# Kernel tuning notes

Measured on AMD Instinct MI355X. Metric: run time of the kernel, lower is better.

## Reference

```python
import jax, jax.numpy as jnp
import numpy as np

EPS = 1e-8
H, DH = 4, 8
HID = H * DH  # 32
FF = 20       # 4 * dim
C = 5         # channels per degree


def snorm(x):
    # grad-safe L2 norm over last axis
    return jnp.sqrt(jnp.sum(x * x, axis=-1) + 1e-12)


def _ln(v, gamma, beta):
    mu = v.mean(-1, keepdims=True)
    sd = v.std(-1, keepdims=True) + EPS
    return (v - mu) / sd * gamma + beta


def norm_se3(x0, x1, g, b):
    # equivariant norm: transform per-channel invariant norms, keep orientation (phase)
    n0 = jnp.abs(x0)
    y0 = jnp.sign(x0) * jax.nn.gelu(_ln(n0, g[0], b[0]))
    n1 = snorm(x1)                                        # (b,n,c)
    y1 = x1 / n1[..., None] * jax.nn.gelu(_ln(n1, g[1], b[1]))[..., None]
    return y0, y1


def attention(x0, x1, coors, adjm, Wq, Mk, Mv, R1, rb1, R2, rb2, Wo0, Wo1):
    b, n, c = x0.shape
    rel = coors[:, None, :, :] - coors[:, :, None, :]     # (b,i,j,3): x_j - x_i
    dist = jnp.sqrt(jnp.sum(rel * rel, -1, keepdims=True) + 1e-12)
    u = rel / dist                                        # unit directions
    # radial net -> per-edge kernel coefficients for each degree-pair/basis (k and v)
    phi = jax.nn.relu(dist @ R1 + rb1) @ R2 + rb2         # (b,i,j,12*HID)
    (k00, k10, k01, kI, kU, kX, v00, v10, v01, vI, vU, vX) = jnp.split(phi, 12, -1)

    def edge_feats(M, p00, p10, p01, pI, pU, pX):
        y00 = jnp.einsum('bjc,ch->bjh', x0, M[0])
        y10 = jnp.einsum('bjcm,ch->bjhm', x1, M[1])
        y01 = jnp.einsum('bjc,ch->bjh', x0, M[2])
        yI = jnp.einsum('bjcm,ch->bjhm', x1, M[3])
        yU = jnp.einsum('bjcm,ch->bjhm', x1, M[4])
        yX = jnp.einsum('bjcm,ch->bjhm', x1, M[5])
        # degree-0 messages: (0->0) scalar and (1->0) vector.dot(u) paths
        e0 = p00 * y00[:, None] + p10 * jnp.einsum('bjhm,bijm->bijh', y10, u)
        un = u[:, :, :, None, :]                          # (b,i,j,1,3)
        # degree-1 messages: closed-form equivariant bases u*s, I, u(u.v), u x v
        e1 = (p01[..., None] * y01[:, None, :, :, None] * un
              + pI[..., None] * yI[:, None]
              + pU[..., None] * jnp.einsum('bjhm,bijm->bijh', yU, u)[..., None] * un
              + pX[..., None] * jnp.cross(un, yX[:, None]))
        return e0, e1

    k0, k1 = edge_feats(Mk, k00, k10, k01, kI, kU, kX)
    v0, v1 = edge_feats(Mv, v00, v10, v01, vI, vU, vX)

    q0 = jnp.einsum('bic,ch->bih', x0, Wq[0]).reshape(b, n, H, DH)
    q1 = jnp.einsum('bicm,ch->bihm', x1, Wq[1]).reshape(b, n, H, DH, 3)
    logits = (jnp.einsum('bihd,bijhd->bhij', q0, k0.reshape(b, n, n, H, DH))
              + jnp.einsum('bihdm,bijhdm->bhij', q1, k1.reshape(b, n, n, H, DH, 3)))
    logits = logits / jnp.asarray(DH, x0.dtype) ** 0.5
    logits = jnp.where(adjm[:, None], logits, -1e9)       # sparse-neighbor mask
    attn = jax.nn.softmax(logits, axis=-1)
    o0 = jnp.einsum('bhij,bijhd->bihd', attn, v0.reshape(b, n, n, H, DH)).reshape(b, n, HID)
    o1 = jnp.einsum('bhij,bijhdm->bihdm', attn, v1.reshape(b, n, n, H, DH, 3)).reshape(b, n, HID, 3)
    return o0 @ Wo0, jnp.einsum('bnhm,hc->bncm', o1, Wo1)


def feedforward(x0, x1, Wf1, Wf2, gs, bs):
    h0 = jax.nn.gelu(jnp.einsum('bnc,cf->bnf', x0, Wf1[0]))
    h1 = jnp.einsum('bncm,cf->bnfm', x1, Wf1[1])
    h1 = h1 * jax.nn.sigmoid(snorm(h1) * gs + bs)[..., None]   # norm-gated nonlin (equivariant)
    return jnp.einsum('bnf,fc->bnc', h0, Wf2[0]), jnp.einsum('bnfm,fc->bncm', h1, Wf2[1])


def _forward(feats, coors, adj_mat, Wq, Mk, Mv, R1, rb1, R2, rb2, Wo0, Wo1, gnA, bnA, gnF, bnF, Wf1, Wf2, gs, bs, Wh1, bh1, Wh2, bh2):
    b, n, _ = feats.shape
    a = adj_mat.astype(jnp.float32)
    # num_adj_degrees=2: attend over 1-hop OR 2-hop neighbors (plus self)
    adjm = adj_mat | ((a @ a) > 0) | jnp.eye(n, dtype=bool)
    x0 = feats
    x1 = jnp.zeros(feats.shape + (3,), feats.dtype)       # input fiber has only degree-0
    x0n, x1n = norm_se3(x0, x1, gnA, bnA)
    d0, d1 = attention(x0n, x1n, coors, adjm, Wq, Mk, Mv, R1, rb1, R2, rb2, Wo0, Wo1)
    x0, x1 = x0 + d0, x1 + d1
    x0n, x1n = norm_se3(x0, x1, gnF, bnF)
    f0, f1 = feedforward(x0n, x1n, Wf1, Wf2, gs, bs)
    x0, x1 = x0 + f0, x1 + f1
    pooled = x0.mean(axis=1)                              # mean pool type-0 features
    h = jax.nn.relu(pooled @ Wh1 + bh1)
    out = h @ Wh2 + bh2                                   # (b, 9)
    return out.reshape(-1, 3, 3)


def setup_inputs():
    key = jax.random.key(0)
    ks = jax.random.split(key, 16)
    B, N = 2, 256
    g = lambda i, shape, s: jax.random.normal(ks[i], shape, jnp.float32) * s
    feats = g(0, (B, N, C), 1.0)
    coors = g(1, (B, N, 3), 3.0)
    r = jax.random.uniform(ks[2], (B, N, N))
    adj = r < 0.03
    adj = (adj | jnp.swapaxes(adj, 1, 2)) & ~jnp.eye(N, dtype=bool)
    s5, sh, sf, s128 = C ** -0.5, HID ** -0.5, FF ** -0.5, 128 ** -0.5
    return dict(
        feats=feats, coors=coors, adj_mat=adj,
        Wq=g(3, (2, C, HID), s5), Mk=g(4, (6, C, HID), s5), Mv=g(5, (6, C, HID), s5),
        R1=g(6, (1, 32), 1.0), rb1=jnp.zeros(32), R2=g(7, (32, 12 * HID), 32 ** -0.5), rb2=jnp.zeros(12 * HID),
        Wo0=g(8, (HID, C), sh), Wo1=g(9, (HID, C), sh),
        gnA=jnp.ones((2, C)), bnA=jnp.zeros((2, C)), gnF=jnp.ones((2, C)), bnF=jnp.zeros((2, C)),
        Wf1=g(10, (2, C, FF), s5), Wf2=g(11, (2, FF, C), sf), gs=jnp.ones(FF), bs=jnp.zeros(FF),
        Wh1=g(12, (C, 128), s5), bh1=jnp.zeros(128), Wh2=g(13, (128, 9), s128), bh2=jnp.zeros(9))


def reference(feats, coors, adj_mat, Wq, Mk, Mv, R1, rb1, R2, rb2, Wo0, Wo1, gnA, bnA, gnF, bnF, Wf1, Wf2, gs, bs, Wh1, bh1, Wh2, bh2):
    return _forward(feats, coors, adj_mat, Wq, Mk, Mv, R1, rb1, R2, rb2, Wo0, Wo1, gnA, bnA, gnF, bnF, Wf1, Wf2, gs, bs, Wh1, bh1, Wh2, bh2)
```

## Files before the change

kernel.cpp:

```cpp
#include <hip/hip_runtime.h>
#include <math.h>

#define BB 2
#define NN 256
#define CC 5
#define HIDD 32


__device__ __forceinline__ float gelu_tanh(float x) {
    float x3 = x * x * x;
    return 0.5f * x * (1.0f + tanhf(0.7978845608028654f * (x + 0.044715f * x3)));
}
__device__ __forceinline__ float sgnf(float x) {
    return (x > 0.f) ? 1.f : ((x < 0.f) ? -1.f : 0.f);
}

#define TROW 9
#define TSZ (33 * TROW)

__global__ __launch_bounds__(256) void prep(
    const int* __restrict__ adj,
    const float* __restrict__ feats,
    const float* __restrict__ Wq0, const float* __restrict__ Mk0, const float* __restrict__ Mv0,
    const float* __restrict__ gnA0, const float* __restrict__ bnA0,
    const float* __restrict__ R1, const float* __restrict__ rb1,
    const float* __restrict__ R2, const float* __restrict__ rb2,
    unsigned long long* __restrict__ bits,
    float* __restrict__ q0, float* __restrict__ yk, float* __restrict__ yv,
    float* __restrict__ table,
    float* __restrict__ tsg)
{
    int bid = blockIdx.x;
    int tid = threadIdx.x;

    if (bid < 128) {
        int lane = tid & 63, wave = tid >> 6;
        int row = bid * 4 + wave;
#pragma unroll
        for (int k = 0; k < 4; k++) {
            int v = adj[(size_t)row * NN + k * 64 + lane];
            unsigned long long m = __ballot(v != 0);
            if (lane == 0) bits[row * 4 + k] = m;
        }
    } else if (bid < 192) {
        int node = (bid - 128) * 8 + (tid >> 5);
        int hd = tid & 31;
        const float* f = feats + node * CC;
        float n0[CC], x0n[CC];
        float mu = 0.f;
#pragma unroll
        for (int c = 0; c < CC; c++) { n0[c] = fabsf(f[c]); mu += n0[c]; }
        mu *= (1.0f / CC);
        float var = 0.f;
#pragma unroll
        for (int c = 0; c < CC; c++) { float d = n0[c] - mu; var += d * d; }
        var *= (1.0f / CC);
        float sd = sqrtf(var) + 1e-8f;
#pragma unroll
        for (int c = 0; c < CC; c++) {
            float ln = (n0[c] - mu) / sd * gnA0[c] + bnA0[c];
            x0n[c] = sgnf(f[c]) * gelu_tanh(ln);
        }
        float q = 0.f, k = 0.f, v = 0.f;
#pragma unroll
        for (int c = 0; c < CC; c++) {
            q = fmaf(x0n[c], Wq0[c * HIDD + hd], q);
            k = fmaf(x0n[c], Mk0[c * HIDD + hd], k);
            v = fmaf(x0n[c], Mv0[c * HIDD + hd], v);
        }
        q0[node * HIDD + hd] = q;
        yk[node * HIDD + hd] = k;
        yv[node * HIDD + hd] = v;
    } else {
        __shared__ float sR1[32], srb1[32], tt[32], ts[32], reps[33];
        if (tid < 32) { sR1[tid] = R1[tid]; srb1[tid] = rb1[tid]; }
        __syncthreads();
        if (tid < 32) {
            float r = sR1[tid];
            tt[tid] = (r != 0.f) ? (-srb1[tid] / r) : -3.0e38f;
        }
        __syncthreads();
        if (tid < 32) {
            float t = tt[tid];
            int rank = 0;
            for (int k = 0; k < 32; k++) {
                float tk = tt[k];
                rank += (tk < t) || (tk == t && k < tid);
            }
            ts[rank] = t;
        }
        __syncthreads();
        if (tid < 33) {
            float rep;
            if (tid == 0) rep = ts[0] - 1.0f;
            else if (tid == 32) rep = ts[31] + 1.0f;
            else rep = 0.5f * (ts[tid - 1] + ts[tid]);
            reps[tid] = rep;
            if (tid < 32) tsg[tid] = ts[tid];
        }
        __syncthreads();
        for (int idx = tid; idx < 33 * 32; idx += 256) {
            int p = idx >> 5, hd = idx & 31;
            float rep = reps[p];
            float A = 0.f, Bv = 0.f, Cv = 0.f, Dv = 0.f;
            for (int w = 0; w < 32; w++) {
                float r = sR1[w], bb = srb1[w];
                if (fmaf(r, rep, bb) > 0.f) {
                    float rk = R2[w * 384 + hd];
                    float rv = R2[w * 384 + 192 + hd];
                    A = fmaf(r, rk, A); Bv = fmaf(bb, rk, Bv);
                    Cv = fmaf(r, rv, Cv); Dv = fmaf(bb, rv, Dv);
                }
            }
            Bv += rb2[hd];
            Dv += rb2[192 + hd];
            table[0 * 33 * 36 + p * 36 + hd] = A;
            table[1 * 33 * 36 + p * 36 + hd] = Bv;
            table[2 * 33 * 36 + p * 36 + hd] = Cv;
            table[3 * 33 * 36 + p * 36 + hd] = Dv;
        }
    }
}

__global__ __launch_bounds__(256) void edge_attn(
    const float* __restrict__ coors,
    const float* __restrict__ q0g, const float* __restrict__ ykg, const float* __restrict__ yvg,
    const unsigned long long* __restrict__ bits,
    const float* __restrict__ feats,
    const float* __restrict__ Wo0,
    const float* __restrict__ gnF0, const float* __restrict__ bnF0,
    const float* __restrict__ Wf10,
    const float* __restrict__ Wf20,
    const float* __restrict__ table, const float* __restrict__ tsg,
    float* __restrict__ xfin)
{
    int node = blockIdx.x;
    int b = node >> 8, i = node & 255;
    int tid = threadIdx.x;
    int j = tid;
    int lane = tid & 63, wave = tid >> 6;

    __shared__ float4 sT[4 * TSZ];
    __shared__ float sts[32], q0s[32];
    __shared__ float Wo0t[5][32];
    __shared__ unsigned long long sbits[4];
    __shared__ float wredm[4][4], wreds[4][4], hm[4], hs[4];
    __shared__ float ew[4][5], x0as[5], xfs[5], h0s[20];

    {
        const float4* tg = (const float4*)table;
        for (int idx = tid; idx < 4 * TSZ; idx += 256) sT[idx] = tg[idx];
    }
    if (tid < 32) { sts[tid] = tsg[tid]; q0s[tid] = q0g[node * 32 + tid]; }
    if (tid < 160) Wo0t[tid / 32][tid % 32] = Wo0[(tid % 32) * 5 + tid / 32];
    if (tid < 4) sbits[tid] = bits[node * 4 + tid];
    __syncthreads();

    float dx = coors[(b * NN + j) * 3 + 0] - coors[(b * NN + i) * 3 + 0];
    float dy = coors[(b * NN + j) * 3 + 1] - coors[(b * NN + i) * 3 + 1];
    float dz = coors[(b * NN + j) * 3 + 2] - coors[(b * NN + i) * 3 + 2];
    float dist = sqrtf(dx * dx + dy * dy + dz * dz + 1e-12f);

    int p = 0;
#pragma unroll
    for (int k = 0; k < 32; k++) p += (sts[k] < dist) ? 1 : 0;

    const float4* Ap = sT + 0 * TSZ + p * TROW;
    const float4* Bp = sT + 1 * TSZ + p * TROW;
    const float4* Cp = sT + 2 * TSZ + p * TROW;
    const float4* Dp = sT + 3 * TSZ + p * TROW;
    const float4* ykp = (const float4*)(ykg + (size_t)(b * NN + j) * 32);
    const float4* yvp = (const float4*)(yvg + (size_t)(b * NN + j) * 32);
    const float4* q04 = (const float4*)q0s;

    float lg[4] = {0.f, 0.f, 0.f, 0.f};
#pragma unroll
    for (int q = 0; q < 8; q++) {
        float4 a = Ap[q], bb = Bp[q], y = ykp[q], qq = q04[q];
        int h = q >> 1;
        lg[h] = fmaf(fmaf(dist, a.x, bb.x) * qq.x, y.x, lg[h]);
        lg[h] = fmaf(fmaf(dist, a.y, bb.y) * qq.y, y.y, lg[h]);
        lg[h] = fmaf(fmaf(dist, a.z, bb.z) * qq.z, y.z, lg[h]);
        lg[h] = fmaf(fmaf(dist, a.w, bb.w) * qq.w, y.w, lg[h]);
    }

    {
        const unsigned long long* myb = bits + (size_t)(b * NN + j) * 4;
        bool direct = (sbits[j >> 6] >> (j & 63)) & 1ull;
        unsigned long long shr = (sbits[0] & myb[0]) | (sbits[1] & myb[1]) |
                                 (sbits[2] & myb[2]) | (sbits[3] & myb[3]);
        bool ok = direct || (shr != 0ull) || (i == j);
        const float invs = 0.35355339059327379f;
#pragma unroll
        for (int h = 0; h < 4; h++) lg[h] = ok ? lg[h] * invs : -1e9f;
    }

    float attn[4];
#pragma unroll
    for (int h = 0; h < 4; h++) {
        float v = lg[h];
        for (int off = 32; off; off >>= 1) v = fmaxf(v, __shfl_xor(v, off, 64));
        if (lane == 0) wredm[h][wave] = v;
    }
    __syncthreads();
    if (tid < 4) hm[tid] = fmaxf(fmaxf(wredm[tid][0], wredm[tid][1]), fmaxf(wredm[tid][2], wredm[tid][3]));
    __syncthreads();
#pragma unroll
    for (int h = 0; h < 4; h++) lg[h] = expf(lg[h] - hm[h]);
#pragma unroll
    for (int h = 0; h < 4; h++) {
        float v = lg[h];
        for (int off = 32; off; off >>= 1) v += __shfl_xor(v, off, 64);
        if (lane == 0) wreds[h][wave] = v;
    }
    __syncthreads();
    if (tid < 4) hs[tid] = wreds[tid][0] + wreds[tid][1] + wreds[tid][2] + wreds[tid][3];
    __syncthreads();
#pragma unroll
    for (int h = 0; h < 4; h++) attn[h] = lg[h] / hs[h];

    float e[5] = {0.f, 0.f, 0.f, 0.f, 0.f};
#pragma unroll
    for (int q = 0; q < 8; q++) {
        float4 c4 = Cp[q], d4 = Dp[q], y = yvp[q];
        float at = attn[q >> 1];
        float4 pv;
        pv.x = at * fmaf(dist, c4.x, d4.x) * y.x;
        pv.y = at * fmaf(dist, c4.y, d4.y) * y.y;
        pv.z = at * fmaf(dist, c4.z, d4.z) * y.z;
        pv.w = at * fmaf(dist, c4.w, d4.w) * y.w;
#pragma unroll
        for (int c = 0; c < 5; c++) {
            float4 w4 = ((const float4*)Wo0t[c])[q];
            e[c] = fmaf(pv.x, w4.x, fmaf(pv.y, w4.y, fmaf(pv.z, w4.z, fmaf(pv.w, w4.w, e[c]))));
        }
    }
    for (int off = 32; off; off >>= 1)
#pragma unroll
        for (int c = 0; c < 5; c++) e[c] += __shfl_xor(e[c], off, 64);
    if (lane == 0)
#pragma unroll
        for (int c = 0; c < 5; c++) ew[wave][c] = e[c];
    __syncthreads();

    if (tid < 5) {
        float d0 = ew[0][tid] + ew[1][tid] + ew[2][tid] + ew[3][tid];
        x0as[tid] = feats[node * 5 + tid] + d0;
    }
    __syncthreads();
    if (tid < 5) {
        float x0a[5], n0[5];
        float mu = 0.f;
#pragma unroll
        for (int c = 0; c < 5; c++) { x0a[c] = x0as[c]; n0[c] = fabsf(x0a[c]); mu += n0[c]; }
        mu *= 0.2f;
        float var = 0.f;
#pragma unroll
        for (int c = 0; c < 5; c++) { float d = n0[c] - mu; var += d * d; }
        var *= 0.2f;
        float sd = sqrtf(var) + 1e-8f;
        float ln = (n0[tid] - mu) / sd * gnF0[tid] + bnF0[tid];
        xfs[tid] = sgnf(x0a[tid]) * gelu_tanh(ln);
    }
    __syncthreads();
    if (tid < 20) {
        float s = 0.f;
#pragma unroll
        for (int c = 0; c < 5; c++) s = fmaf(xfs[c], Wf10[c * 20 + tid], s);
        h0s[tid] = gelu_tanh(s);
    }
    __syncthreads();
    if (tid < 5) {
        float f0 = 0.f;
        for (int f = 0; f < 20; f++) f0 = fmaf(h0s[f], Wf20[f * 5 + tid], f0);
        xfin[node * 5 + tid] = x0as[tid] + f0;
    }
}

__global__ __launch_bounds__(256) void head_mlp(const float* __restrict__ xfin,
                         const float* __restrict__ Wh1, const float* __restrict__ bh1,
                         const float* __restrict__ Wh2, const float* __restrict__ bh2,
                         float* __restrict__ out) {
    __shared__ float part[2][5][25];
    __shared__ float pooled[10];
    __shared__ float hdn[2][128];
    int tid = threadIdx.x;
    if (tid < 250) {
        int b = tid / 125, r = tid % 125, c = r / 25, grp = r % 25;
        float s = 0.f;
        for (int i = grp; i < NN; i += 25) s += xfin[(b * NN + i) * 5 + c];
        part[b][c][grp] = s;
    }
    __syncthreads();
    if (tid < 10) {
        int b = tid / 5, c = tid % 5;
        float s = 0.f;
        for (int g = 0; g < 25; g++) s += part[b][c][g];
        pooled[tid] = s * (1.0f / NN);
    }
    __syncthreads();
    {
        int b = tid >> 7, k = tid & 127;
        float s = bh1[k];
#pragma unroll
        for (int c = 0; c < 5; c++) s = fmaf(pooled[b * 5 + c], Wh1[c * 128 + k], s);
        hdn[b][k] = fmaxf(s, 0.f);
    }
    __syncthreads();
    if (tid < 18) {
        int b = tid / 9, o = tid % 9;
        float s = bh2[o];
        for (int k = 0; k < 128; k++) s = fmaf(hdn[b][k], Wh2[k * 9 + o], s);
        out[b * 9 + o] = s;
    }
}

extern "C" void kernel_launch(void* const* d_in, const int* in_sizes, int n_in,
                              void* d_out, int out_size, void* d_ws, size_t ws_size,
                              hipStream_t stream) {
    const float* feats = (const float*)d_in[0];
    const float* coors = (const float*)d_in[1];
    const int*   adj   = (const int*)d_in[2];
    const float* Wq    = (const float*)d_in[3];
    const float* Mk    = (const float*)d_in[4];
    const float* Mv    = (const float*)d_in[5];
    const float* R1    = (const float*)d_in[6];
    const float* rb1   = (const float*)d_in[7];
    const float* R2    = (const float*)d_in[8];
    const float* rb2   = (const float*)d_in[9];
    const float* Wo0   = (const float*)d_in[10];
    const float* gnA   = (const float*)d_in[12];
    const float* bnA   = (const float*)d_in[13];
    const float* gnF   = (const float*)d_in[14];
    const float* bnF   = (const float*)d_in[15];
    const float* Wf1   = (const float*)d_in[16];
    const float* Wf2   = (const float*)d_in[17];
    const float* Wh1   = (const float*)d_in[20];
    const float* bh1   = (const float*)d_in[21];
    const float* Wh2   = (const float*)d_in[22];
    const float* bh2   = (const float*)d_in[23];
    float* out = (float*)d_out;

    float* q0    = (float*)d_ws;
    float* yk    = q0 + 512 * 32;
    float* yv    = yk + 512 * 32;
    float* xfin  = yv + 512 * 32;
    float* tsg   = xfin + 512 * 8;
    unsigned long long* bits = (unsigned long long*)(tsg + 32);
    float* table = (float*)(bits + 512 * 4);

    hipLaunchKernelGGL(prep, dim3(193), dim3(256), 0, stream,
                       adj, feats, Wq, Mk, Mv, gnA, bnA, R1, rb1, R2, rb2,
                       bits, q0, yk, yv, table, tsg);
    hipLaunchKernelGGL(edge_attn, dim3(512), dim3(256), 0, stream,
                       coors, q0, yk, yv, bits, feats, Wo0, gnF, bnF, Wf1, Wf2,
                       table, tsg, xfin);
    hipLaunchKernelGGL(head_mlp, dim3(1), dim3(256), 0, stream,
                       xfin, Wh1, bh1, Wh2, bh2, out);
}
```

Baseline: 133.8 us.

## Fuse head MLP into edge kernel via last-block atomic pooling; read table from global

```diff
diff --git a/kernel.cpp b/kernel.cpp
--- a/kernel.cpp
+++ b/kernel.cpp
@@ -14,9 +14,6 @@
 __device__ __forceinline__ float sgnf(float x) {
     return (x > 0.f) ? 1.f : ((x < 0.f) ? -1.f : 0.f);
 }
-
-#define TROW 9
-#define TSZ (33 * TROW)
 
 __global__ __launch_bounds__(256) void prep(
     const int* __restrict__ adj,
@@ -28,7 +25,9 @@
     unsigned long long* __restrict__ bits,
     float* __restrict__ q0, float* __restrict__ yk, float* __restrict__ yv,
     float* __restrict__ table,
-    float* __restrict__ tsg)
+    float* __restrict__ tsg,
+    float* __restrict__ pooled,
+    unsigned int* __restrict__ counter)
 {
     int bid = blockIdx.x;
     int tid = threadIdx.x;
@@ -73,6 +72,8 @@
         yv[node * HIDD + hd] = v;
     } else {
         __shared__ float sR1[32], srb1[32], tt[32], ts[32], reps[33];
+        if (tid < 16) pooled[tid] = 0.f;
+        if (tid == 16) *counter = 0u;
         if (tid < 32) { sR1[tid] = R1[tid]; srb1[tid] = rb1[tid]; }
         __syncthreads();
         if (tid < 32) {
@@ -132,7 +133,10 @@
     const float* __restrict__ Wf10,
     const float* __restrict__ Wf20,
     const float* __restrict__ table, const float* __restrict__ tsg,
-    float* __restrict__ xfin)
+    const float* __restrict__ Wh1, const float* __restrict__ bh1,
+    const float* __restrict__ Wh2, const float* __restrict__ bh2,
+    float* __restrict__ pooled, unsigned int* __restrict__ counter,
+    float* __restrict__ out)
 {
     int node = blockIdx.x;
     int b = node >> 8, i = node & 255;
@@ -140,20 +144,19 @@
     int j = tid;
     int lane = tid & 63, wave = tid >> 6;
 
-    __shared__ float4 sT[4 * TSZ];
     __shared__ float sts[32], q0s[32];
     __shared__ float Wo0t[5][32];
     __shared__ unsigned long long sbits[4];
     __shared__ float wredm[4][4], wreds[4][4], hm[4], hs[4];
     __shared__ float ew[4][5], x0as[5], xfs[5], h0s[20];
-
-    {
-        const float4* tg = (const float4*)table;
-        for (int idx = tid; idx < 4 * TSZ; idx += 256) sT[idx] = tg[idx];
-    }
+    __shared__ int lastflag;
+    __shared__ float pl[10];
+    __shared__ float hdn[2][128];
+
     if (tid < 32) { sts[tid] = tsg[tid]; q0s[tid] = q0g[node * 32 + tid]; }
     if (tid < 160) Wo0t[tid / 32][tid % 32] = Wo0[(tid % 32) * 5 + tid / 32];
     if (tid < 4) sbits[tid] = bits[node * 4 + tid];
+    if (tid == 0) lastflag = 0;
     __syncthreads();
 
     float dx = coors[(b * NN + j) * 3 + 0] - coors[(b * NN + i) * 3 + 0];
@@ -165,10 +168,10 @@
 #pragma unroll
     for (int k = 0; k < 32; k++) p += (sts[k] < dist) ? 1 : 0;
 
-    const float4* Ap = sT + 0 * TSZ + p * TROW;
-    const float4* Bp = sT + 1 * TSZ + p * TROW;
-    const float4* Cp = sT + 2 * TSZ + p * TROW;
-    const float4* Dp = sT + 3 * TSZ + p * TROW;
+    const float4* Ap = (const float4*)(table + 0 * 33 * 36 + p * 36);
+    const float4* Bp = (const float4*)(table + 1 * 33 * 36 + p * 36);
+    const float4* Cp = (const float4*)(table + 2 * 33 * 36 + p * 36);
+    const float4* Dp = (const float4*)(table + 3 * 33 * 36 + p * 36);
     const float4* ykp = (const float4*)(ykg + (size_t)(b * NN + j) * 32);
     const float4* yvp = (const float4*)(yvg + (size_t)(b * NN + j) * 32);
     const float4* q04 = (const float4*)q0s;
@@ -176,7 +179,7 @@
     float lg[4] = {0.f, 0.f, 0.f, 0.f};
 #pragma unroll
     for (int q = 0; q < 8; q++) {
-        float4 a = Ap[q], bb = Bp[q], y = ykp[q], qq = q04[q];
+        float4 a = __ldg(&Ap[q]), bb = __ldg(&Bp[q]), y = ykp[q], qq = q04[q];
         int h = q >> 1;
         lg[h] = fmaf(fmaf(dist, a.x, bb.x) * qq.x, y.x, lg[h]);
         lg[h] = fmaf(fmaf(dist, a.y, bb.y) * qq.y, y.y, lg[h]);
@@ -222,7 +225,7 @@
     float e[5] = {0.f, 0.f, 0.f, 0.f, 0.f};
 #pragma unroll
     for (int q = 0; q < 8; q++) {
-        float4 c4 = Cp[q], d4 = Dp[q], y = yvp[q];
+        float4 c4 = __ldg(&Cp[q]), d4 = __ldg(&Dp[q]), y = yvp[q];
         float at = attn[q >> 1];
         float4 pv;
         pv.x = at * fmaf(dist, c4.x, d4.x) * y.x;
@@ -273,45 +276,34 @@
     if (tid < 5) {
         float f0 = 0.f;
         for (int f = 0; f < 20; f++) f0 = fmaf(h0s[f], Wf20[f * 5 + tid], f0);
-        xfin[node * 5 + tid] = x0as[tid] + f0;
-    }
-}
-
-__global__ __launch_bounds__(256) void head_mlp(const float* __restrict__ xfin,
-                         const float* __restrict__ Wh1, const float* __restrict__ bh1,
-                         const float* __restrict__ Wh2, const float* __restrict__ bh2,
-                         float* __restrict__ out) {
-    __shared__ float part[2][5][25];
-    __shared__ float pooled[10];
-    __shared__ float hdn[2][128];
-    int tid = threadIdx.x;
-    if (tid < 250) {
-        int b = tid / 125, r = tid % 125, c = r / 25, grp = r % 25;
-        float s = 0.f;
-        for (int i = grp; i < NN; i += 25) s += xfin[(b * NN + i) * 5 + c];
-        part[b][c][grp] = s;
-    }
-    __syncthreads();
-    if (tid < 10) {
-        int b = tid / 5, c = tid % 5;
-        float s = 0.f;
-        for (int g = 0; g < 25; g++) s += part[b][c][g];
-        pooled[tid] = s * (1.0f / NN);
-    }
-    __syncthreads();
-    {
-        int b = tid >> 7, k = tid & 127;
-        float s = bh1[k];
-#pragma unroll
-        for (int c = 0; c < 5; c++) s = fmaf(pooled[b * 5 + c], Wh1[c * 128 + k], s);
-        hdn[b][k] = fmaxf(s, 0.f);
-    }
-    __syncthreads();
-    if (tid < 18) {
-        int b = tid / 9, o = tid % 9;
-        float s = bh2[o];
-        for (int k = 0; k < 128; k++) s = fmaf(hdn[b][k], Wh2[k * 9 + o], s);
-        out[b * 9 + o] = s;
+        atomicAdd(&pooled[b * 5 + tid], x0as[tid] + f0);
+        __threadfence();
+    }
+    __syncthreads();
+    if (tid == 0) {
+        unsigned int old = atomicAdd(counter, 1u);
+        if (old == (unsigned int)(gridDim.x - 1)) lastflag = 1;
+    }
+    __syncthreads();
+
+    if (lastflag) {
+        if (tid < 10) pl[tid] = atomicAdd(&pooled[tid], 0.f);
+        __syncthreads();
+        {
+            int bb2 = tid >> 7, k = tid & 127;
+            float s = bh1[k];
+#pragma unroll
+            for (int c = 0; c < 5; c++)
+                s = fmaf(pl[bb2 * 5 + c] * (1.0f / NN), Wh1[c * 128 + k], s);
+            hdn[bb2][k] = fmaxf(s, 0.f);
+        }
+        __syncthreads();
+        if (tid < 18) {
+            int bb2 = tid / 9, o = tid % 9;
+            float s = bh2[o];
+            for (int k = 0; k < 128; k++) s = fmaf(hdn[bb2][k], Wh2[k * 9 + o], s);
+            out[bb2 * 9 + o] = s;
+        }
     }
 }
 
@@ -344,17 +336,16 @@
     float* q0    = (float*)d_ws;
     float* yk    = q0 + 512 * 32;
     float* yv    = yk + 512 * 32;
-    float* xfin  = yv + 512 * 32;
-    float* tsg   = xfin + 512 * 8;
-    unsigned long long* bits = (unsigned long long*)(tsg + 32);
-    float* table = (float*)(bits + 512 * 4);
+    float* table = yv + 512 * 32;
+    float* tsg   = table + 4 * 33 * 36;
+    float* pooled = tsg + 32;
+    unsigned int* counter = (unsigned int*)(pooled + 16);
+    unsigned long long* bits = (unsigned long long*)(pooled + 20);
 
     hipLaunchKernelGGL(prep, dim3(193), dim3(256), 0, stream,
                        adj, feats, Wq, Mk, Mv, gnA, bnA, R1, rb1, R2, rb2,
-                       bits, q0, yk, yv, table, tsg);
+                       bits, q0, yk, yv, table, tsg, pooled, counter);
     hipLaunchKernelGGL(edge_attn, dim3(512), dim3(256), 0, stream,
                        coors, q0, yk, yv, bits, feats, Wo0, gnF, bnF, Wf1, Wf2,
-                       table, tsg, xfin);
-    hipLaunchKernelGGL(head_mlp, dim3(1), dim3(256), 0, stream,
-                       xfin, Wh1, bh1, Wh2, bh2, out);
-}
+                       table, tsg, Wh1, bh1, Wh2, bh2, pooled, counter, out);
+}
```

Measured after the change: 137.0 us. +2.4%, slower.
